# Kernel tuning notes

Measured on AMD Instinct MI355X. Metric: run time of the kernel, lower is better.

Reference implementation:

```python
import jax, jax.numpy as jnp
import numpy as np

B, S, IN_DIM, D_MODEL, H = 1, 4096, 512, 512, 8
DK = D_MODEL // H


def setup_inputs() -> dict:
    key = jax.random.key(0)
    ks = jax.random.split(key, 10)
    sc_in = 1.0 / np.sqrt(IN_DIM)
    sc_dm = 1.0 / np.sqrt(D_MODEL)
    return {
        "x": jax.random.normal(ks[0], (B, S, IN_DIM), dtype=jnp.float32),
        "mask": jax.random.randint(ks[1], (1, 1, S, S), 0, 2, dtype=jnp.int32),
        "wq_w": jax.random.uniform(ks[2], (D_MODEL, IN_DIM), jnp.float32, -sc_in, sc_in),
        "wq_b": jax.random.uniform(ks[3], (D_MODEL,), jnp.float32, -sc_in, sc_in),
        "wk_w": jax.random.uniform(ks[4], (D_MODEL, IN_DIM), jnp.float32, -sc_in, sc_in),
        "wk_b": jax.random.uniform(ks[5], (D_MODEL,), jnp.float32, -sc_in, sc_in),
        "wv_w": jax.random.uniform(ks[6], (D_MODEL, IN_DIM), jnp.float32, -sc_in, sc_in),
        "wv_b": jax.random.uniform(ks[7], (D_MODEL,), jnp.float32, -sc_in, sc_in),
        "dense_w": jax.random.uniform(ks[8], (D_MODEL, D_MODEL), jnp.float32, -sc_dm, sc_dm),
        "dense_b": jax.random.uniform(ks[9], (D_MODEL,), jnp.float32, -sc_dm, sc_dm),
    }


def _split_heads(t):
    # Faithful to original: raw view [B, S, D] -> [B, H, S, DK] (no transpose)
    return t.reshape(B, H, S, DK)


def reference(x, mask, wq_w, wq_b, wk_w, wk_b, wv_w, wv_b, dense_w, dense_b):
    q = _split_heads(x @ wq_w.T + wq_b)  # [B, H, S, DK]
    k = _split_heads(x @ wk_w.T + wk_b)
    v = _split_heads(x @ wv_w.T + wv_b)
    score = jnp.einsum("bhqd,bhkd->bhqk", q, k) / np.sqrt(DK).astype(np.float32)
    score = score + mask.astype(score.dtype) * (-1e9)
    attn = jax.nn.softmax(score, axis=-1)
    out = jnp.einsum("bhqk,bhkd->bhqd", attn, v)  # [B, H, S, DK]
    out = out.transpose(0, 2, 1, 3).reshape(B, S, D_MODEL)
    return out @ dense_w.T + dense_b
```

## Files before the change

kernel.cpp:

```cpp
#include <hip/hip_runtime.h>
#include <hip/hip_bf16.h>

#define S_LEN 4096
#define DM    512
#define NH    8
#define DK    64

typedef __attribute__((ext_vector_type(8))) __bf16 bf16x8;
typedef __attribute__((ext_vector_type(4))) float  f32x4;
typedef unsigned short u16;
typedef unsigned int   u32;
typedef unsigned long long u64;

#define SQ_SCALE (0.125f * 1.44269504f)
#define FMAX 12.0f

__device__ __forceinline__ u16 f2bf(float f) {
  union { float f; u32 i; } v; v.f = f;
  u32 r = v.i + 0x7fff + ((v.i >> 16) & 1);
  return (u16)(r >> 16);
}
__device__ __forceinline__ float bf2f(u16 u) {
  union { u32 i; float f; } v; v.i = ((u32)u) << 16; return v.f;
}

__global__ __launch_bounds__(256) void pack_mask(const int* __restrict__ mask,
                                                 u64* __restrict__ out) {
  int gid = blockIdx.x * 256 + threadIdx.x;
  u64 b = __ballot(mask[gid] != 0);
  if ((threadIdx.x & 63) == 0) out[gid >> 6] = b;
}

__global__ __launch_bounds__(256) void convert_all(
    const float* __restrict__ x, const float* __restrict__ wq,
    const float* __restrict__ wk, const float* __restrict__ wv,
    const float* __restrict__ dw,
    u16* __restrict__ xb, u16* __restrict__ wcat, u16* __restrict__ dwb) {
  int b = blockIdx.x;
  const float* src; u16* dst; size_t off;
  if      (b < 2048) { src = x;  dst = xb;   off = (size_t)b * 1024; }
  else if (b < 2304) { src = wq; dst = wcat; off = (size_t)(b - 2048) * 1024; }
  else if (b < 2560) { src = wk; dst = wcat + 262144; off = (size_t)(b - 2304) * 1024; }
  else if (b < 2816) { src = wv; dst = wcat + 524288; off = (size_t)(b - 2560) * 1024; }
  else               { src = dw; dst = dwb;  off = (size_t)(b - 2816) * 1024; }
  size_t i = off + (size_t)threadIdx.x * 4;
  float4 v = *reinterpret_cast<const float4*>(src + i);
  ushort4 o = make_ushort4(f2bf(v.x), f2bf(v.y), f2bf(v.z), f2bf(v.w));
  *reinterpret_cast<ushort4*>(dst + i) = o;
}

__global__ __launch_bounds__(256) void qkv_gemm(
    const u16* __restrict__ A, const u16* __restrict__ Wcat,
    const float* __restrict__ bq, const float* __restrict__ bk,
    const float* __restrict__ bv,
    u16* __restrict__ Qb, u16* __restrict__ Kb, u16* __restrict__ V4) {
  __shared__ u16 As[64 * 72];
  __shared__ u16 Ws[128 * 72];
  const int t = threadIdx.x;
  const int lane = t & 63, wv = t >> 6;
  const int m16 = lane & 15, quad = lane >> 4;
  const int n0g = blockIdx.x * 128, m0 = blockIdx.y * 64;
  const int seg = n0g >> 9;
  const int n0 = n0g & 511;
  const int mq = wv >> 1, nq = wv & 1;

  f32x4 acc[2][4];
#pragma unroll
  for (int i = 0; i < 2; i++)
#pragma unroll
    for (int j = 0; j < 4; j++) acc[i][j] = (f32x4)0.f;

  for (int k0 = 0; k0 < DM; k0 += 64) {
    __syncthreads();
#pragma unroll
    for (int c0 = 0; c0 < 2; c0++) {
      int c = t + c0 * 256;
      int row = c >> 3, col = (c & 7) * 8;
      *reinterpret_cast<uint4*>(&As[row * 72 + col]) =
          *reinterpret_cast<const uint4*>(&A[(size_t)(m0 + row) * DM + k0 + col]);
    }
#pragma unroll
    for (int c0 = 0; c0 < 4; c0++) {
      int c = t + c0 * 256;
      int row = c >> 3, col = (c & 7) * 8;
      *reinterpret_cast<uint4*>(&Ws[row * 72 + col]) =
          *reinterpret_cast<const uint4*>(&Wcat[(size_t)(n0g + row) * DM + k0 + col]);
    }
    __syncthreads();
#pragma unroll
    for (int kk = 0; kk < 64; kk += 32) {
      bf16x8 a0 = *reinterpret_cast<const bf16x8*>(&As[(mq * 32 + m16) * 72 + quad * 8 + kk]);
      bf16x8 a1 = *reinterpret_cast<const bf16x8*>(&As[(mq * 32 + 16 + m16) * 72 + quad * 8 + kk]);
#pragma unroll
      for (int ct = 0; ct < 4; ct++) {
        bf16x8 b = *reinterpret_cast<const bf16x8*>(&Ws[(nq * 64 + ct * 16 + m16) * 72 + quad * 8 + kk]);
        acc[0][ct] = __builtin_amdgcn_mfma_f32_16x16x32_bf16(a0, b, acc[0][ct], 0, 0, 0);
        acc[1][ct] = __builtin_amdgcn_mfma_f32_16x16x32_bf16(a1, b, acc[1][ct], 0, 0, 0);
      }
    }
  }

  const float* bias = (seg == 0) ? bq : (seg == 1) ? bk : bv;
  const float scale = (seg == 0) ? SQ_SCALE : 1.f;
  float bn[4];
#pragma unroll
  for (int ct = 0; ct < 4; ct++) bn[ct] = bias[n0 + nq * 64 + ct * 16 + m16];

  if (seg == 2) {
    __syncthreads();
    u16* T = Ws;
#pragma unroll
    for (int rt = 0; rt < 2; rt++)
#pragma unroll
      for (int ct = 0; ct < 4; ct++)
#pragma unroll
        for (int r = 0; r < 4; r++)
          T[(nq * 64 + ct * 16 + m16) * 72 + mq * 32 + rt * 16 + quad * 4 + r] =
              f2bf(acc[rt][ct][r] + bn[ct]);
    __syncthreads();
    const int h    = m0 >> 9;
    const int mp   = m0 & 511;
    const int cseg = n0 >> 7;
#pragma unroll
    for (int c0 = 0; c0 < 4; c0++) {
      int c = t + c0 * 256;
      int d  = c >> 4;
      int tl = (c >> 1) & 7;
      int cl = c & 1;
      uint4 v = *reinterpret_cast<const uint4*>(&T[(cl * 64 + d) * 72 + tl * 8]);
      *reinterpret_cast<uint4*>(
          &V4[(size_t)(h * 64 + d) * 4096 + ((mp >> 3) + tl) * 64 + cl * 32 + cseg * 8]) = v;
    }
  } else {
    u16* dst = (seg == 0) ? Qb : Kb;
#pragma unroll
    for (int rt = 0; rt < 2; rt++)
#pragma unroll
      for (int ct = 0; ct < 4; ct++) {
        int n = n0 + nq * 64 + ct * 16 + m16;
#pragma unroll
        for (int r = 0; r < 4; r++) {
          int m = m0 + mq * 32 + rt * 16 + quad * 4 + r;
          dst[(size_t)m * DM + n] = f2bf((acc[rt][ct][r] + bn[ct]) * scale);
        }
      }
  }
}

__global__ __launch_bounds__(256) void dense_gemm(
    const u16* __restrict__ A, const u16* __restrict__ W,
    const float* __restrict__ bias, float* __restrict__ Cout) {
  __shared__ u16 As[64 * 72];
  __shared__ u16 Ws[64 * 72];
  const int t = threadIdx.x;
  const int lane = t & 63, wv = t >> 6;
  const int m16 = lane & 15, quad = lane >> 4;
  const int n0 = blockIdx.x * 64, m0 = blockIdx.y * 64;

  f32x4 acc[4];
#pragma unroll
  for (int j = 0; j < 4; j++) acc[j] = (f32x4)0.f;

  for (int k0 = 0; k0 < DM; k0 += 64) {
    __syncthreads();
#pragma unroll
    for (int c0 = 0; c0 < 2; c0++) {
      int c = t + c0 * 256;
      int row = c >> 3, col = (c & 7) * 8;
      *reinterpret_cast<uint4*>(&As[row * 72 + col]) =
          *reinterpret_cast<const uint4*>(&A[(size_t)(m0 + row) * DM + k0 + col]);
      *reinterpret_cast<uint4*>(&Ws[row * 72 + col]) =
          *reinterpret_cast<const uint4*>(&W[(size_t)(n0 + row) * DM + k0 + col]);
    }
    __syncthreads();
#pragma unroll
    for (int kk = 0; kk < 64; kk += 32) {
      bf16x8 a = *reinterpret_cast<const bf16x8*>(&As[(wv * 16 + m16) * 72 + quad * 8 + kk]);
#pragma unroll
      for (int ct = 0; ct < 4; ct++) {
        bf16x8 b = *reinterpret_cast<const bf16x8*>(&Ws[(ct * 16 + m16) * 72 + quad * 8 + kk]);
        acc[ct] = __builtin_amdgcn_mfma_f32_16x16x32_bf16(a, b, acc[ct], 0, 0, 0);
      }
    }
  }

  float bn[4];
#pragma unroll
  for (int ct = 0; ct < 4; ct++) bn[ct] = bias[n0 + ct * 16 + m16];
#pragma unroll
  for (int ct = 0; ct < 4; ct++) {
    int n = n0 + ct * 16 + m16;
#pragma unroll
    for (int r = 0; r < 4; r++) {
      int m = m0 + wv * 16 + quad * 4 + r;
      Cout[(size_t)m * DM + n] = acc[ct][r] + bn[ct];
    }
  }
}

__device__ __forceinline__ void pack_p(const f32x4* s, u32 lo, u32 hi,
                                       uint4& o0, uint4& o1) {
  u32 pk[8];
#pragma unroll
  for (int ct = 0; ct < 4; ct++) {
    u32 w = (ct & 1) ? hi : lo;
    int b = ct >> 1;
    float p0 = __builtin_amdgcn_exp2f(((w >> b) & 1u)        ? -1e9f : s[ct][0]);
    float p1 = __builtin_amdgcn_exp2f(((w >> (b + 8)) & 1u)  ? -1e9f : s[ct][1]);
    float p2 = __builtin_amdgcn_exp2f(((w >> (b + 16)) & 1u) ? -1e9f : s[ct][2]);
    float p3 = __builtin_amdgcn_exp2f(((w >> (b + 24)) & 1u) ? -1e9f : s[ct][3]);
    pk[2 * ct]     = __builtin_amdgcn_perm(__float_as_uint(p1) + 0x8000u,
                                           __float_as_uint(p0) + 0x8000u, 0x07060302u);
    pk[2 * ct + 1] = __builtin_amdgcn_perm(__float_as_uint(p3) + 0x8000u,
                                           __float_as_uint(p2) + 0x8000u, 0x07060302u);
  }
  o0 = make_uint4(pk[0], pk[1], pk[2], pk[3]);
  o1 = make_uint4(pk[4], pk[5], pk[6], pk[7]);
}

__global__ __launch_bounds__(256, 4) void attn_mfma(
    const u16* __restrict__ Q, const u16* __restrict__ K,
    const u16* __restrict__ V4, const u64* __restrict__ mbits,
    u16* __restrict__ Op, float* __restrict__ Lp) {
  __shared__ u16 Ks[64 * 72];
  __shared__ u16 Vs[64 * 72];

  const int t = threadIdx.x;
  const int lane = t & 63, w4 = t >> 6;
  const int m16 = lane & 15, quad = lane >> 4;
  const int q0 = blockIdx.x * 128;
  const int h = blockIdx.y;
  const int g = blockIdx.z;
  const size_t hoff = (size_t)h * S_LEN * DK;
  const size_t kbase = hoff + (size_t)g * 1024 * DK;

  const u16* qpA = Q + hoff + (size_t)(q0 + w4 * 32 + m16) * DK + quad * 8;
  bf16x8 qloA = *reinterpret_cast<const bf16x8*>(qpA);
  bf16x8 qhiA = *reinterpret_cast<const bf16x8*>(qpA + 32);
  bf16x8 qloB = *reinterpret_cast<const bf16x8*>(qpA + 16 * DK);
  bf16x8 qhiB = *reinterpret_cast<const bf16x8*>(qpA + 16 * DK + 32);

  union { u16 u[8]; bf16x8 v; } onesu;
#pragma unroll
  for (int j = 0; j < 8; j++) onesu.u[j] = 0x3F80;
  const bf16x8 ones = onesu.v;

  f32x4 accA[4], accB[4];
  f32x4 acc_lA = (f32x4)0.f, acc_lB = (f32x4)0.f;
#pragma unroll
  for (int dt = 0; dt < 4; dt++) { accA[dt] = (f32x4)0.f; accB[dt] = (f32x4)0.f; }

  for (int k0 = 0; k0 < 1024; k0 += 64) {
    const int kg = g * 1024 + k0;
#pragma unroll
    for (int c0 = 0; c0 < 2; c0++) {
      int c = t + c0 * 256;
      int rg = c >> 3, cc = c & 7;
      int sr = ((rg & 1) << 5) | (((rg >> 5) & 1) << 4) | (((rg >> 2) & 1) << 3) |
               (((rg >> 1) & 1) << 2) | (((rg >> 4) & 1) << 1) | ((rg >> 3) & 1);
      *reinterpret_cast<uint4*>(&Ks[sr * 72 + cc * 8]) =
          *reinterpret_cast<const uint4*>(&K[kbase + (size_t)(k0 + rg) * DK + cc * 8]);
      *reinterpret_cast<uint4*>(&Vs[rg * 72 + cc * 8]) =
          *reinterpret_cast<const uint4*>(&V4[(size_t)(h * 64 + rg) * 4096 + kg + cc * 8]);
    }
    u64 mqA = mbits[(size_t)(q0 + w4 * 32 + m16) * 64 + (kg >> 6)] >> (2 * quad);
    u64 mqB = mbits[(size_t)(q0 + w4 * 32 + 16 + m16) * 64 + (kg >> 6)] >> (2 * quad);
    __syncthreads();

    f32x4 sA[4], sB[4];
#pragma unroll
    for (int ct = 0; ct < 4; ct++) { sA[ct] = (f32x4)(-FMAX); sB[ct] = (f32x4)(-FMAX); }
#pragma unroll
    for (int ct = 0; ct < 4; ct++) {
      bf16x8 klo = *reinterpret_cast<const bf16x8*>(&Ks[(ct * 16 + m16) * 72 + quad * 8]);
      bf16x8 khi = *reinterpret_cast<const bf16x8*>(&Ks[(ct * 16 + m16) * 72 + quad * 8 + 32]);
      sA[ct] = __builtin_amdgcn_mfma_f32_16x16x32_bf16(klo, qloA, sA[ct], 0, 0, 0);
      sA[ct] = __builtin_amdgcn_mfma_f32_16x16x32_bf16(khi, qhiA, sA[ct], 0, 0, 0);
      sB[ct] = __builtin_amdgcn_mfma_f32_16x16x32_bf16(klo, qloB, sB[ct], 0, 0, 0);
      sB[ct] = __builtin_amdgcn_mfma_f32_16x16x32_bf16(khi, qhiB, sB[ct], 0, 0, 0);
    }

    union { uint4 i; bf16x8 v; } pA0, pA1, pB0, pB1;
    pack_p(sA, (u32)mqA, (u32)(mqA >> 32), pA0.i, pA1.i);
    pack_p(sB, (u32)mqB, (u32)(mqB >> 32), pB0.i, pB1.i);

#pragma unroll
    for (int dt = 0; dt < 4; dt++) {
      bf16x8 vlo = *reinterpret_cast<const bf16x8*>(&Vs[(dt * 16 + m16) * 72 + quad * 8]);
      bf16x8 vhi = *reinterpret_cast<const bf16x8*>(&Vs[(dt * 16 + m16) * 72 + quad * 8 + 32]);
      accA[dt] = __builtin_amdgcn_mfma_f32_16x16x32_bf16(pA0.v, vlo, accA[dt], 0, 0, 0);
      accA[dt] = __builtin_amdgcn_mfma_f32_16x16x32_bf16(pA1.v, vhi, accA[dt], 0, 0, 0);
      accB[dt] = __builtin_amdgcn_mfma_f32_16x16x32_bf16(pB0.v, vlo, accB[dt], 0, 0, 0);
      accB[dt] = __builtin_amdgcn_mfma_f32_16x16x32_bf16(pB1.v, vhi, accB[dt], 0, 0, 0);
    }
    acc_lA = __builtin_amdgcn_mfma_f32_16x16x32_bf16(pA0.v, ones, acc_lA, 0, 0, 0);
    acc_lA = __builtin_amdgcn_mfma_f32_16x16x32_bf16(pA1.v, ones, acc_lA, 0, 0, 0);
    acc_lB = __builtin_amdgcn_mfma_f32_16x16x32_bf16(pB0.v, ones, acc_lB, 0, 0, 0);
    acc_lB = __builtin_amdgcn_mfma_f32_16x16x32_bf16(pB1.v, ones, acc_lB, 0, 0, 0);
    __syncthreads();
  }

  u16* Og = Op + (size_t)g * 2097152;
#pragma unroll
  for (int dt = 0; dt < 4; dt++)
#pragma unroll
    for (int r = 0; r < 4; r++) {
      Og[(size_t)(q0 + w4 * 32 + quad * 4 + r) * DM + h * DK + dt * 16 + m16] =
          f2bf(accA[dt][r]);
      Og[(size_t)(q0 + w4 * 32 + 16 + quad * 4 + r) * DM + h * DK + dt * 16 + m16] =
          f2bf(accB[dt][r]);
    }
  if (m16 == 0) {
#pragma unroll
    for (int r = 0; r < 4; r++) {
      Lp[g * 32768 + h * 4096 + q0 + w4 * 32 + quad * 4 + r] = acc_lA[r];
      Lp[g * 32768 + h * 4096 + q0 + w4 * 32 + 16 + quad * 4 + r] = acc_lB[r];
    }
  }
}

__global__ __launch_bounds__(256) void attn_merge(
    const u16* __restrict__ Op, const float* __restrict__ Lp,
    u16* __restrict__ Out) {
  int i8 = (blockIdx.x * 256 + threadIdx.x) * 8;
  int q = i8 >> 9;
  int h = (i8 >> 6) & 7;
  float l = 0.f;
#pragma unroll
  for (int part = 0; part < 4; part++) l += Lp[part * 32768 + h * 4096 + q];
  float rl = 1.f / l;
  float o[8];
#pragma unroll
  for (int j = 0; j < 8; j++) o[j] = 0.f;
#pragma unroll
  for (int part = 0; part < 4; part++) {
    ushort4 v0 = *reinterpret_cast<const ushort4*>(Op + part * 2097152 + i8);
    ushort4 v1 = *reinterpret_cast<const ushort4*>(Op + part * 2097152 + i8 + 4);
    o[0] += bf2f(v0.x); o[1] += bf2f(v0.y); o[2] += bf2f(v0.z); o[3] += bf2f(v0.w);
    o[4] += bf2f(v1.x); o[5] += bf2f(v1.y); o[6] += bf2f(v1.z); o[7] += bf2f(v1.w);
  }
  ushort4 o0 = make_ushort4(f2bf(o[0] * rl), f2bf(o[1] * rl),
                            f2bf(o[2] * rl), f2bf(o[3] * rl));
  ushort4 o1 = make_ushort4(f2bf(o[4] * rl), f2bf(o[5] * rl),
                            f2bf(o[6] * rl), f2bf(o[7] * rl));
  *reinterpret_cast<ushort4*>(Out + i8) = o0;
  *reinterpret_cast<ushort4*>(Out + i8 + 4) = o1;
}

extern "C" void kernel_launch(void* const* d_in, const int* in_sizes, int n_in,
                              void* d_out, int out_size, void* d_ws, size_t ws_size,
                              hipStream_t stream) {
  const float* x    = (const float*)d_in[0];
  const int*   mask = (const int*)d_in[1];
  const float* wq_w = (const float*)d_in[2];
  const float* wq_b = (const float*)d_in[3];
  const float* wk_w = (const float*)d_in[4];
  const float* wk_b = (const float*)d_in[5];
  const float* wv_w = (const float*)d_in[6];
  const float* wv_b = (const float*)d_in[7];
  const float* dw   = (const float*)d_in[8];
  const float* db   = (const float*)d_in[9];

  u16* xb    = (u16*)d_ws;
  u16* wcat  = xb    + 2097152;
  u16* dwb   = wcat  + 786432;
  u16* Qb    = dwb   + 262144;
  u16* Kb    = Qb    + 2097152;
  u16* V4    = Kb    + 2097152;
  u16* Opart = V4    + 2097152;
  u64* mb    = (u64*)(Opart + 4 * 2097152);
  float* Lp  = (float*)(mb + 262144);

  pack_mask<<<(S_LEN * S_LEN) / 256, 256, 0, stream>>>(mask, mb);
  convert_all<<<3072, 256, 0, stream>>>(x, wq_w, wk_w, wv_w, dw, xb, wcat, dwb);

  qkv_gemm<<<dim3(12, 64), 256, 0, stream>>>(xb, wcat, wq_b, wk_b, wv_b,
                                             Qb, Kb, V4);

  attn_mfma<<<dim3(32, NH, 4), 256, 0, stream>>>(Qb, Kb, V4, mb, Opart, Lp);
  attn_merge<<<1024, 256, 0, stream>>>(Opart, Lp, Qb);

  dense_gemm<<<dim3(8, 64), 256, 0, stream>>>(Qb, dwb, db, (float*)d_out);
}
```

Before: 225.4 us.

## Merge mask packing with conversion; load GEMM weight fragments directly from global

Combines the mask bit-packing and fp32-to-bf16 conversion kernels into one launch, with each mask block now handling 16 chunks. In both GEMMs the weight operand is no longer staged through LDS; each lane reads its bf16x8 B fragment straight from global memory, which cuts LDS traffic and the shared-memory footprint. The V transpose epilogue is reworked into two passes through a smaller LDS buffer. The cost is uncoalesced, cache-dependent global reads for the weights inside the MFMA loop, plus extra barriers in the V epilogue.

```diff
diff --git a/kernel.cpp b/kernel.cpp
--- a/kernel.cpp
+++ b/kernel.cpp
@@ -24,29 +24,33 @@
   union { u32 i; float f; } v; v.i = ((u32)u) << 16; return v.f;
 }
 
-__global__ __launch_bounds__(256) void pack_mask(const int* __restrict__ mask,
-                                                 u64* __restrict__ out) {
-  int gid = blockIdx.x * 256 + threadIdx.x;
-  u64 b = __ballot(mask[gid] != 0);
-  if ((threadIdx.x & 63) == 0) out[gid >> 6] = b;
-}
-
-__global__ __launch_bounds__(256) void convert_all(
+__global__ __launch_bounds__(256) void prep(
+    const int* __restrict__ mask, u64* __restrict__ mb,
     const float* __restrict__ x, const float* __restrict__ wq,
     const float* __restrict__ wk, const float* __restrict__ wv,
     const float* __restrict__ dw,
     u16* __restrict__ xb, u16* __restrict__ wcat, u16* __restrict__ dwb) {
   int b = blockIdx.x;
-  const float* src; u16* dst; size_t off;
-  if      (b < 2048) { src = x;  dst = xb;   off = (size_t)b * 1024; }
-  else if (b < 2304) { src = wq; dst = wcat; off = (size_t)(b - 2048) * 1024; }
-  else if (b < 2560) { src = wk; dst = wcat + 262144; off = (size_t)(b - 2304) * 1024; }
-  else if (b < 2816) { src = wv; dst = wcat + 524288; off = (size_t)(b - 2560) * 1024; }
-  else               { src = dw; dst = dwb;  off = (size_t)(b - 2816) * 1024; }
-  size_t i = off + (size_t)threadIdx.x * 4;
-  float4 v = *reinterpret_cast<const float4*>(src + i);
-  ushort4 o = make_ushort4(f2bf(v.x), f2bf(v.y), f2bf(v.z), f2bf(v.w));
-  *reinterpret_cast<ushort4*>(dst + i) = o;
+  if (b < 4096) {
+#pragma unroll
+    for (int i = 0; i < 16; i++) {
+      int gid = (b * 16 + i) * 256 + threadIdx.x;
+      u64 bb = __ballot(mask[gid] != 0);
+      if ((threadIdx.x & 63) == 0) mb[gid >> 6] = bb;
+    }
+  } else {
+    b -= 4096;
+    const float* src; u16* dst; size_t off;
+    if      (b < 2048) { src = x;  dst = xb;   off = (size_t)b * 1024; }
+    else if (b < 2304) { src = wq; dst = wcat; off = (size_t)(b - 2048) * 1024; }
+    else if (b < 2560) { src = wk; dst = wcat + 262144; off = (size_t)(b - 2304) * 1024; }
+    else if (b < 2816) { src = wv; dst = wcat + 524288; off = (size_t)(b - 2560) * 1024; }
+    else               { src = dw; dst = dwb;  off = (size_t)(b - 2816) * 1024; }
+    size_t i = off + (size_t)threadIdx.x * 4;
+    float4 v = *reinterpret_cast<const float4*>(src + i);
+    ushort4 o = make_ushort4(f2bf(v.x), f2bf(v.y), f2bf(v.z), f2bf(v.w));
+    *reinterpret_cast<ushort4*>(dst + i) = o;
+  }
 }
 
 __global__ __launch_bounds__(256) void qkv_gemm(
@@ -55,7 +59,7 @@
     const float* __restrict__ bv,
     u16* __restrict__ Qb, u16* __restrict__ Kb, u16* __restrict__ V4) {
   __shared__ u16 As[64 * 72];
-  __shared__ u16 Ws[128 * 72];
+  __shared__ u16 T[64 * 72];
   const int t = threadIdx.x;
   const int lane = t & 63, wv = t >> 6;
   const int m16 = lane & 15, quad = lane >> 4;
@@ -70,6 +74,8 @@
 #pragma unroll
     for (int j = 0; j < 4; j++) acc[i][j] = (f32x4)0.f;
 
+  const u16* wrow = Wcat + (size_t)(n0g + nq * 64 + m16) * DM + quad * 8;
+
   for (int k0 = 0; k0 < DM; k0 += 64) {
     __syncthreads();
 #pragma unroll
@@ -79,13 +85,6 @@
       *reinterpret_cast<uint4*>(&As[row * 72 + col]) =
           *reinterpret_cast<const uint4*>(&A[(size_t)(m0 + row) * DM + k0 + col]);
     }
-#pragma unroll
-    for (int c0 = 0; c0 < 4; c0++) {
-      int c = t + c0 * 256;
-      int row = c >> 3, col = (c & 7) * 8;
-      *reinterpret_cast<uint4*>(&Ws[row * 72 + col]) =
-          *reinterpret_cast<const uint4*>(&Wcat[(size_t)(n0g + row) * DM + k0 + col]);
-    }
     __syncthreads();
 #pragma unroll
     for (int kk = 0; kk < 64; kk += 32) {
@@ -93,7 +92,7 @@
       bf16x8 a1 = *reinterpret_cast<const bf16x8*>(&As[(mq * 32 + 16 + m16) * 72 + quad * 8 + kk]);
 #pragma unroll
       for (int ct = 0; ct < 4; ct++) {
-        bf16x8 b = *reinterpret_cast<const bf16x8*>(&Ws[(nq * 64 + ct * 16 + m16) * 72 + quad * 8 + kk]);
+        bf16x8 b = *reinterpret_cast<const bf16x8*>(wrow + (size_t)ct * 16 * DM + k0 + kk);
         acc[0][ct] = __builtin_amdgcn_mfma_f32_16x16x32_bf16(a0, b, acc[0][ct], 0, 0, 0);
         acc[1][ct] = __builtin_amdgcn_mfma_f32_16x16x32_bf16(a1, b, acc[1][ct], 0, 0, 0);
       }
@@ -107,29 +106,31 @@
   for (int ct = 0; ct < 4; ct++) bn[ct] = bias[n0 + nq * 64 + ct * 16 + m16];
 
   if (seg == 2) {
-    __syncthreads();
-    u16* T = Ws;
-#pragma unroll
-    for (int rt = 0; rt < 2; rt++)
-#pragma unroll
-      for (int ct = 0; ct < 4; ct++)
-#pragma unroll
-        for (int r = 0; r < 4; r++)
-          T[(nq * 64 + ct * 16 + m16) * 72 + mq * 32 + rt * 16 + quad * 4 + r] =
-              f2bf(acc[rt][ct][r] + bn[ct]);
-    __syncthreads();
     const int h    = m0 >> 9;
     const int mp   = m0 & 511;
     const int cseg = n0 >> 7;
 #pragma unroll
-    for (int c0 = 0; c0 < 4; c0++) {
-      int c = t + c0 * 256;
-      int d  = c >> 4;
-      int tl = (c >> 1) & 7;
-      int cl = c & 1;
-      uint4 v = *reinterpret_cast<const uint4*>(&T[(cl * 64 + d) * 72 + tl * 8]);
-      *reinterpret_cast<uint4*>(
-          &V4[(size_t)(h * 64 + d) * 4096 + ((mp >> 3) + tl) * 64 + cl * 32 + cseg * 8]) = v;
+    for (int p = 0; p < 2; p++) {
+      if (nq == p) {
+#pragma unroll
+        for (int rt = 0; rt < 2; rt++)
+#pragma unroll
+          for (int ct = 0; ct < 4; ct++)
+#pragma unroll
+            for (int r = 0; r < 4; r++)
+              T[(ct * 16 + m16) * 72 + mq * 32 + rt * 16 + quad * 4 + r] =
+                  f2bf(acc[rt][ct][r] + bn[ct]);
+      }
+      __syncthreads();
+#pragma unroll
+      for (int c0 = 0; c0 < 2; c0++) {
+        int c = t + c0 * 256;
+        int row = c >> 3, tl = c & 7;
+        *reinterpret_cast<uint4*>(
+            &V4[(size_t)(h * 64 + row) * 4096 + ((mp >> 3) + tl) * 64 + p * 32 + cseg * 8]) =
+            *reinterpret_cast<const uint4*>(&T[row * 72 + tl * 8]);
+      }
+      __syncthreads();
     }
   } else {
     u16* dst = (seg == 0) ? Qb : Kb;
@@ -151,7 +152,6 @@
     const u16* __restrict__ A, const u16* __restrict__ W,
     const float* __restrict__ bias, float* __restrict__ Cout) {
   __shared__ u16 As[64 * 72];
-  __shared__ u16 Ws[64 * 72];
   const int t = threadIdx.x;
   const int lane = t & 63, wv = t >> 6;
   const int m16 = lane & 15, quad = lane >> 4;
@@ -160,6 +160,8 @@
   f32x4 acc[4];
 #pragma unroll
   for (int j = 0; j < 4; j++) acc[j] = (f32x4)0.f;
+
+  const u16* wrow = W + (size_t)(n0 + m16) * DM + quad * 8;
 
   for (int k0 = 0; k0 < DM; k0 += 64) {
     __syncthreads();
@@ -169,8 +171,6 @@
       int row = c >> 3, col = (c & 7) * 8;
       *reinterpret_cast<uint4*>(&As[row * 72 + col]) =
           *reinterpret_cast<const uint4*>(&A[(size_t)(m0 + row) * DM + k0 + col]);
-      *reinterpret_cast<uint4*>(&Ws[row * 72 + col]) =
-          *reinterpret_cast<const uint4*>(&W[(size_t)(n0 + row) * DM + k0 + col]);
     }
     __syncthreads();
 #pragma unroll
@@ -178,7 +178,7 @@
       bf16x8 a = *reinterpret_cast<const bf16x8*>(&As[(wv * 16 + m16) * 72 + quad * 8 + kk]);
 #pragma unroll
       for (int ct = 0; ct < 4; ct++) {
-        bf16x8 b = *reinterpret_cast<const bf16x8*>(&Ws[(ct * 16 + m16) * 72 + quad * 8 + kk]);
+        bf16x8 b = *reinterpret_cast<const bf16x8*>(wrow + (size_t)ct * 16 * DM + k0 + kk);
         acc[ct] = __builtin_amdgcn_mfma_f32_16x16x32_bf16(a, b, acc[ct], 0, 0, 0);
       }
     }
@@ -371,8 +371,8 @@
   u64* mb    = (u64*)(Opart + 4 * 2097152);
   float* Lp  = (float*)(mb + 262144);
 
-  pack_mask<<<(S_LEN * S_LEN) / 256, 256, 0, stream>>>(mask, mb);
-  convert_all<<<3072, 256, 0, stream>>>(x, wq_w, wk_w, wv_w, dw, xb, wcat, dwb);
+  prep<<<7168, 256, 0, stream>>>(mask, mb, x, wq_w, wk_w, wv_w, dw,
+                                 xb, wcat, dwb);
 
   qkv_gemm<<<dim3(12, 64), 256, 0, stream>>>(xb, wcat, wq_b, wk_b, wv_b,
                                              Qb, Kb, V4);
```

After: 242.3 us. 1.07x slower.

## Fuse conversions, mask packing and merge into the QKV and dense GEMM kernels

Applied to the files above, without the earlier changes.

Removes the separate fp32-to-bf16 conversion kernel by converting x and the weights while staging tiles into shared memory inside the GEMMs. Mask bit-packing is folded into the QKV launch as extra blocks, and the split-K attention merge (partial-sum reduction plus 1/l normalization) is folded into the dense GEMM's A-tile load. This drops three launches and the intermediate bf16 buffers, at the cost of GEMMs that re-read and re-convert fp32 data per tile and a dense GEMM that reads four partial outputs for every tile.

```diff
diff --git a/kernel.cpp b/kernel.cpp
--- a/kernel.cpp
+++ b/kernel.cpp
@@ -23,46 +23,43 @@
 __device__ __forceinline__ float bf2f(u16 u) {
   union { u32 i; float f; } v; v.i = ((u32)u) << 16; return v.f;
 }
-
-__global__ __launch_bounds__(256) void pack_mask(const int* __restrict__ mask,
-                                                 u64* __restrict__ out) {
-  int gid = blockIdx.x * 256 + threadIdx.x;
-  u64 b = __ballot(mask[gid] != 0);
-  if ((threadIdx.x & 63) == 0) out[gid >> 6] = b;
-}
-
-__global__ __launch_bounds__(256) void convert_all(
-    const float* __restrict__ x, const float* __restrict__ wq,
-    const float* __restrict__ wk, const float* __restrict__ wv,
-    const float* __restrict__ dw,
-    u16* __restrict__ xb, u16* __restrict__ wcat, u16* __restrict__ dwb) {
-  int b = blockIdx.x;
-  const float* src; u16* dst; size_t off;
-  if      (b < 2048) { src = x;  dst = xb;   off = (size_t)b * 1024; }
-  else if (b < 2304) { src = wq; dst = wcat; off = (size_t)(b - 2048) * 1024; }
-  else if (b < 2560) { src = wk; dst = wcat + 262144; off = (size_t)(b - 2304) * 1024; }
-  else if (b < 2816) { src = wv; dst = wcat + 524288; off = (size_t)(b - 2560) * 1024; }
-  else               { src = dw; dst = dwb;  off = (size_t)(b - 2816) * 1024; }
-  size_t i = off + (size_t)threadIdx.x * 4;
-  float4 v = *reinterpret_cast<const float4*>(src + i);
-  ushort4 o = make_ushort4(f2bf(v.x), f2bf(v.y), f2bf(v.z), f2bf(v.w));
-  *reinterpret_cast<ushort4*>(dst + i) = o;
-}
-
-__global__ __launch_bounds__(256) void qkv_gemm(
-    const u16* __restrict__ A, const u16* __restrict__ Wcat,
+__device__ __forceinline__ ushort4 cvt4(float4 v) {
+  return make_ushort4(f2bf(v.x), f2bf(v.y), f2bf(v.z), f2bf(v.w));
+}
+
+__global__ __launch_bounds__(256) void qkv_prep(
+    const float* __restrict__ x,
+    const float* __restrict__ wq, const float* __restrict__ wk,
+    const float* __restrict__ wv,
     const float* __restrict__ bq, const float* __restrict__ bk,
     const float* __restrict__ bv,
+    const int* __restrict__ mask, u64* __restrict__ mb,
     u16* __restrict__ Qb, u16* __restrict__ Kb, u16* __restrict__ V4) {
   __shared__ u16 As[64 * 72];
   __shared__ u16 Ws[128 * 72];
   const int t = threadIdx.x;
-  const int lane = t & 63, wv = t >> 6;
+  int b = blockIdx.x;
+
+  if (b >= 768) {
+    int mbb = b - 768;
+#pragma unroll
+    for (int i = 0; i < 16; i++) {
+      int gid = (mbb * 16 + i) * 256 + t;
+      u64 bb = __ballot(mask[gid] != 0);
+      if ((t & 63) == 0) mb[gid >> 6] = bb;
+    }
+    return;
+  }
+
+  const int bx = b % 12, by = b / 12;
+  const int lane = t & 63, wv4 = t >> 6;
   const int m16 = lane & 15, quad = lane >> 4;
-  const int n0g = blockIdx.x * 128, m0 = blockIdx.y * 64;
+  const int n0g = bx * 128, m0 = by * 64;
   const int seg = n0g >> 9;
   const int n0 = n0g & 511;
-  const int mq = wv >> 1, nq = wv & 1;
+  const int mq = wv4 >> 1, nq = wv4 & 1;
+
+  const float* Wsrc = (seg == 0) ? wq : (seg == 1) ? wk : wv;
 
   f32x4 acc[2][4];
 #pragma unroll
@@ -73,18 +70,20 @@
   for (int k0 = 0; k0 < DM; k0 += 64) {
     __syncthreads();
 #pragma unroll
-    for (int c0 = 0; c0 < 2; c0++) {
-      int c = t + c0 * 256;
-      int row = c >> 3, col = (c & 7) * 8;
-      *reinterpret_cast<uint4*>(&As[row * 72 + col]) =
-          *reinterpret_cast<const uint4*>(&A[(size_t)(m0 + row) * DM + k0 + col]);
-    }
-#pragma unroll
     for (int c0 = 0; c0 < 4; c0++) {
       int c = t + c0 * 256;
-      int row = c >> 3, col = (c & 7) * 8;
-      *reinterpret_cast<uint4*>(&Ws[row * 72 + col]) =
-          *reinterpret_cast<const uint4*>(&Wcat[(size_t)(n0g + row) * DM + k0 + col]);
+      int row = c >> 4, col4 = (c & 15) * 4;
+      float4 v = *reinterpret_cast<const float4*>(
+          &x[(size_t)(m0 + row) * DM + k0 + col4]);
+      *reinterpret_cast<ushort4*>(&As[row * 72 + col4]) = cvt4(v);
+    }
+#pragma unroll
+    for (int c0 = 0; c0 < 8; c0++) {
+      int c = t + c0 * 256;
+      int row = c >> 4, col4 = (c & 15) * 4;
+      float4 v = *reinterpret_cast<const float4*>(
+          &Wsrc[(size_t)(n0 + row) * DM + k0 + col4]);
+      *reinterpret_cast<ushort4*>(&Ws[row * 72 + col4]) = cvt4(v);
     }
     __syncthreads();
 #pragma unroll
@@ -93,9 +92,9 @@
       bf16x8 a1 = *reinterpret_cast<const bf16x8*>(&As[(mq * 32 + 16 + m16) * 72 + quad * 8 + kk]);
 #pragma unroll
       for (int ct = 0; ct < 4; ct++) {
-        bf16x8 b = *reinterpret_cast<const bf16x8*>(&Ws[(nq * 64 + ct * 16 + m16) * 72 + quad * 8 + kk]);
-        acc[0][ct] = __builtin_amdgcn_mfma_f32_16x16x32_bf16(a0, b, acc[0][ct], 0, 0, 0);
-        acc[1][ct] = __builtin_amdgcn_mfma_f32_16x16x32_bf16(a1, b, acc[1][ct], 0, 0, 0);
+        bf16x8 bb = *reinterpret_cast<const bf16x8*>(&Ws[(nq * 64 + ct * 16 + m16) * 72 + quad * 8 + kk]);
+        acc[0][ct] = __builtin_amdgcn_mfma_f32_16x16x32_bf16(a0, bb, acc[0][ct], 0, 0, 0);
+        acc[1][ct] = __builtin_amdgcn_mfma_f32_16x16x32_bf16(a1, bb, acc[1][ct], 0, 0, 0);
       }
     }
   }
@@ -144,57 +143,6 @@
           dst[(size_t)m * DM + n] = f2bf((acc[rt][ct][r] + bn[ct]) * scale);
         }
       }
-  }
-}
-
-__global__ __launch_bounds__(256) void dense_gemm(
-    const u16* __restrict__ A, const u16* __restrict__ W,
-    const float* __restrict__ bias, float* __restrict__ Cout) {
-  __shared__ u16 As[64 * 72];
-  __shared__ u16 Ws[64 * 72];
-  const int t = threadIdx.x;
-  const int lane = t & 63, wv = t >> 6;
-  const int m16 = lane & 15, quad = lane >> 4;
-  const int n0 = blockIdx.x * 64, m0 = blockIdx.y * 64;
-
-  f32x4 acc[4];
-#pragma unroll
-  for (int j = 0; j < 4; j++) acc[j] = (f32x4)0.f;
-
-  for (int k0 = 0; k0 < DM; k0 += 64) {
-    __syncthreads();
-#pragma unroll
-    for (int c0 = 0; c0 < 2; c0++) {
-      int c = t + c0 * 256;
-      int row = c >> 3, col = (c & 7) * 8;
-      *reinterpret_cast<uint4*>(&As[row * 72 + col]) =
-          *reinterpret_cast<const uint4*>(&A[(size_t)(m0 + row) * DM + k0 + col]);
-      *reinterpret_cast<uint4*>(&Ws[row * 72 + col]) =
-          *reinterpret_cast<const uint4*>(&W[(size_t)(n0 + row) * DM + k0 + col]);
-    }
-    __syncthreads();
-#pragma unroll
-    for (int kk = 0; kk < 64; kk += 32) {
-      bf16x8 a = *reinterpret_cast<const bf16x8*>(&As[(wv * 16 + m16) * 72 + quad * 8 + kk]);
-#pragma unroll
-      for (int ct = 0; ct < 4; ct++) {
-        bf16x8 b = *reinterpret_cast<const bf16x8*>(&Ws[(ct * 16 + m16) * 72 + quad * 8 + kk]);
-        acc[ct] = __builtin_amdgcn_mfma_f32_16x16x32_bf16(a, b, acc[ct], 0, 0, 0);
-      }
-    }
-  }
-
-  float bn[4];
-#pragma unroll
-  for (int ct = 0; ct < 4; ct++) bn[ct] = bias[n0 + ct * 16 + m16];
-#pragma unroll
-  for (int ct = 0; ct < 4; ct++) {
-    int n = n0 + ct * 16 + m16;
-#pragma unroll
-    for (int r = 0; r < 4; r++) {
-      int m = m0 + wv * 16 + quad * 4 + r;
-      Cout[(size_t)m * DM + n] = acc[ct][r] + bn[ct];
-    }
   }
 }
 
@@ -319,32 +267,88 @@
   }
 }
 
-__global__ __launch_bounds__(256) void attn_merge(
+__global__ __launch_bounds__(256) void dense_merge(
     const u16* __restrict__ Op, const float* __restrict__ Lp,
-    u16* __restrict__ Out) {
-  int i8 = (blockIdx.x * 256 + threadIdx.x) * 8;
-  int q = i8 >> 9;
-  int h = (i8 >> 6) & 7;
-  float l = 0.f;
-#pragma unroll
-  for (int part = 0; part < 4; part++) l += Lp[part * 32768 + h * 4096 + q];
-  float rl = 1.f / l;
-  float o[8];
-#pragma unroll
-  for (int j = 0; j < 8; j++) o[j] = 0.f;
-#pragma unroll
-  for (int part = 0; part < 4; part++) {
-    ushort4 v0 = *reinterpret_cast<const ushort4*>(Op + part * 2097152 + i8);
-    ushort4 v1 = *reinterpret_cast<const ushort4*>(Op + part * 2097152 + i8 + 4);
-    o[0] += bf2f(v0.x); o[1] += bf2f(v0.y); o[2] += bf2f(v0.z); o[3] += bf2f(v0.w);
-    o[4] += bf2f(v1.x); o[5] += bf2f(v1.y); o[6] += bf2f(v1.z); o[7] += bf2f(v1.w);
-  }
-  ushort4 o0 = make_ushort4(f2bf(o[0] * rl), f2bf(o[1] * rl),
-                            f2bf(o[2] * rl), f2bf(o[3] * rl));
-  ushort4 o1 = make_ushort4(f2bf(o[4] * rl), f2bf(o[5] * rl),
-                            f2bf(o[6] * rl), f2bf(o[7] * rl));
-  *reinterpret_cast<ushort4*>(Out + i8) = o0;
-  *reinterpret_cast<ushort4*>(Out + i8 + 4) = o1;
+    const float* __restrict__ W, const float* __restrict__ bias,
+    float* __restrict__ Cout) {
+  __shared__ u16 As[64 * 72];
+  __shared__ u16 Ws[64 * 72];
+  __shared__ float Linv[64 * 8];
+  const int t = threadIdx.x;
+  const int lane = t & 63, wv4 = t >> 6;
+  const int m16 = lane & 15, quad = lane >> 4;
+  const int n0 = blockIdx.x * 64, m0 = blockIdx.y * 64;
+
+#pragma unroll
+  for (int i = 0; i < 2; i++) {
+    int idx = t + i * 256;
+    int m = idx >> 3, h = idx & 7;
+    float l = 0.f;
+#pragma unroll
+    for (int g = 0; g < 4; g++) l += Lp[g * 32768 + h * 4096 + m0 + m];
+    Linv[m * 8 + h] = 1.f / l;
+  }
+
+  f32x4 acc[4];
+#pragma unroll
+  for (int j = 0; j < 4; j++) acc[j] = (f32x4)0.f;
+
+  for (int k0 = 0; k0 < DM; k0 += 64) {
+    const int hh = k0 >> 6;
+    __syncthreads();
+#pragma unroll
+    for (int c0 = 0; c0 < 2; c0++) {
+      int c = t + c0 * 256;
+      int row = c >> 3, col8 = (c & 7) * 8;
+      float o[8];
+#pragma unroll
+      for (int j = 0; j < 8; j++) o[j] = 0.f;
+#pragma unroll
+      for (int g = 0; g < 4; g++) {
+        const u16* p = Op + (size_t)g * 2097152 + (size_t)(m0 + row) * DM + k0 + col8;
+        ushort4 v0 = *reinterpret_cast<const ushort4*>(p);
+        ushort4 v1 = *reinterpret_cast<const ushort4*>(p + 4);
+        o[0] += bf2f(v0.x); o[1] += bf2f(v0.y); o[2] += bf2f(v0.z); o[3] += bf2f(v0.w);
+        o[4] += bf2f(v1.x); o[5] += bf2f(v1.y); o[6] += bf2f(v1.z); o[7] += bf2f(v1.w);
+      }
+      float rl = Linv[row * 8 + hh];
+      *reinterpret_cast<ushort4*>(&As[row * 72 + col8]) =
+          make_ushort4(f2bf(o[0] * rl), f2bf(o[1] * rl), f2bf(o[2] * rl), f2bf(o[3] * rl));
+      *reinterpret_cast<ushort4*>(&As[row * 72 + col8 + 4]) =
+          make_ushort4(f2bf(o[4] * rl), f2bf(o[5] * rl), f2bf(o[6] * rl), f2bf(o[7] * rl));
+    }
+#pragma unroll
+    for (int c0 = 0; c0 < 4; c0++) {
+      int c = t + c0 * 256;
+      int row = c >> 4, col4 = (c & 15) * 4;
+      float4 v = *reinterpret_cast<const float4*>(
+          &W[(size_t)(n0 + row) * DM + k0 + col4]);
+      *reinterpret_cast<ushort4*>(&Ws[row * 72 + col4]) = cvt4(v);
+    }
+    __syncthreads();
+#pragma unroll
+    for (int kk = 0; kk < 64; kk += 32) {
+      bf16x8 a = *reinterpret_cast<const bf16x8*>(&As[(wv4 * 16 + m16) * 72 + quad * 8 + kk]);
+#pragma unroll
+      for (int ct = 0; ct < 4; ct++) {
+        bf16x8 bb = *reinterpret_cast<const bf16x8*>(&Ws[(ct * 16 + m16) * 72 + quad * 8 + kk]);
+        acc[ct] = __builtin_amdgcn_mfma_f32_16x16x32_bf16(a, bb, acc[ct], 0, 0, 0);
+      }
+    }
+  }
+
+  float bn[4];
+#pragma unroll
+  for (int ct = 0; ct < 4; ct++) bn[ct] = bias[n0 + ct * 16 + m16];
+#pragma unroll
+  for (int ct = 0; ct < 4; ct++) {
+    int n = n0 + ct * 16 + m16;
+#pragma unroll
+    for (int r = 0; r < 4; r++) {
+      int m = m0 + wv4 * 16 + quad * 4 + r;
+      Cout[(size_t)m * DM + n] = acc[ct][r] + bn[ct];
+    }
+  }
 }
 
 extern "C" void kernel_launch(void* const* d_in, const int* in_sizes, int n_in,
@@ -361,24 +365,18 @@
   const float* dw   = (const float*)d_in[8];
   const float* db   = (const float*)d_in[9];
 
-  u16* xb    = (u16*)d_ws;
-  u16* wcat  = xb    + 2097152;
-  u16* dwb   = wcat  + 786432;
-  u16* Qb    = dwb   + 262144;
+  u16* Qb    = (u16*)d_ws;
   u16* Kb    = Qb    + 2097152;
   u16* V4    = Kb    + 2097152;
   u16* Opart = V4    + 2097152;
   u64* mb    = (u64*)(Opart + 4 * 2097152);
   float* Lp  = (float*)(mb + 262144);
 
-  pack_mask<<<(S_LEN * S_LEN) / 256, 256, 0, stream>>>(mask, mb);
-  convert_all<<<3072, 256, 0, stream>>>(x, wq_w, wk_w, wv_w, dw, xb, wcat, dwb);
-
-  qkv_gemm<<<dim3(12, 64), 256, 0, stream>>>(xb, wcat, wq_b, wk_b, wv_b,
-                                             Qb, Kb, V4);
+  qkv_prep<<<768 + 4096, 256, 0, stream>>>(x, wq_w, wk_w, wv_w,
+                                           wq_b, wk_b, wv_b,
+                                           mask, mb, Qb, Kb, V4);
 
   attn_mfma<<<dim3(32, NH, 4), 256, 0, stream>>>(Qb, Kb, V4, mb, Opart, Lp);
-  attn_merge<<<1024, 256, 0, stream>>>(Opart, Lp, Qb);
-
-  dense_gemm<<<dim3(8, 64), 256, 0, stream>>>(Qb, dwb, db, (float*)d_out);
-}
+
+  dense_merge<<<dim3(8, 64), 256, 0, stream>>>(Opart, Lp, dw, db, (float*)d_out);
+}
```

After: 279.3 us. 23.9% more time.
